# Kernel optimization log

Measured on AMD Instinct MI355X. Metric: run time of the kernel, lower is better.

The kernel has to match this reference:

```python
import jax, jax.numpy as jnp
import numpy as np

C = 512
NUM_GROUPS = 32
EPS = 1e-6


def group_norm(x, gamma, beta):
    # x: [B, C, H, W]
    B, Cc, H, W = x.shape
    xg = x.reshape(B, NUM_GROUPS, Cc // NUM_GROUPS, H, W)
    mean = xg.mean(axis=(2, 3, 4), keepdims=True)
    var = xg.var(axis=(2, 3, 4), keepdims=True)
    xn = (xg - mean) / jnp.sqrt(var + EPS)
    xn = xn.reshape(B, Cc, H, W)
    return xn * gamma[None, :, None, None] + beta[None, :, None, None]


def conv1x1(x, w, b):
    # w: [out_c, in_c], x: [B, C, H, W]
    return jnp.einsum('oc,bchw->bohw', w, x) + b[None, :, None, None]


def setup_inputs() -> dict:
    key = jax.random.key(0)
    ks = jax.random.split(key, 6)
    B, H, W = 2, 64, 64
    x = jax.random.normal(ks[0], (B, C, H, W), dtype=jnp.float32)
    s = 1.0 / np.sqrt(C)
    wq = jax.random.normal(ks[1], (C, C), dtype=jnp.float32) * s
    wk = jax.random.normal(ks[2], (C, C), dtype=jnp.float32) * s
    wv = jax.random.normal(ks[3], (C, C), dtype=jnp.float32) * s
    wo = jax.random.normal(ks[4], (C, C), dtype=jnp.float32) * s
    bq = jnp.zeros((C,), jnp.float32)
    bk = jnp.zeros((C,), jnp.float32)
    bv = jnp.zeros((C,), jnp.float32)
    bo = jnp.zeros((C,), jnp.float32)
    gamma = jnp.ones((C,), jnp.float32)
    beta = jnp.zeros((C,), jnp.float32)
    return {"x": x, "gamma": gamma, "beta": beta, "wq": wq, "bq": bq,
            "wk": wk, "bk": bk, "wv": wv, "bv": bv, "wo": wo, "bo": bo}


def reference(x, gamma, beta, wq, bq, wk, bk, wv, bv, wo, bo):
    B, Cc, H, W = x.shape
    h = group_norm(x, gamma, beta)
    q = conv1x1(h, wq, bq).reshape(B, Cc, H * W)  # [B, C, N]
    k = conv1x1(h, wk, bk).reshape(B, Cc, H * W)
    v = conv1x1(h, wv, bv).reshape(B, Cc, H * W)
    scale = Cc ** (-0.5)
    # scores a[b,i,j] = sum_c q[b,c,i] * k[b,c,j]
    a = jnp.einsum('bci,bcj->bij', q, k) * scale
    a = jax.nn.softmax(a, axis=2)
    # out[b,c,i] = sum_j v[b,c,j] * a[b,i,j]  (matches bmm(v, a^T))
    o = jnp.einsum('bcj,bij->bci', v, a).reshape(B, Cc, H, W)
    o = conv1x1(o, wo, bo)
    return x + o
```

## Files before the change

kernel.cpp:

```cpp
#include <hip/hip_runtime.h>
#include <stdint.h>

#define NPIX 4096
#define CDIM 512

typedef _Float16 hv8 __attribute__((ext_vector_type(8)));
typedef float f32x4 __attribute__((ext_vector_type(4)));

__device__ __forceinline__ void lds_direct16(const _Float16* g, _Float16* l) {
    __builtin_amdgcn_global_load_lds(
        (const __attribute__((address_space(1))) void*)g,
        (__attribute__((address_space(3))) void*)l, 16, 0, 0);
}

__global__ void cvt_w(const float* __restrict__ s0, const float* __restrict__ s1,
                      const float* __restrict__ s2, const float* __restrict__ s3,
                      _Float16* __restrict__ d0, _Float16* __restrict__ d1,
                      _Float16* __restrict__ d2, _Float16* __restrict__ d3) {
    int i = blockIdx.x * 256 + threadIdx.x;
    d0[i] = (_Float16)s0[i];
    d1[i] = (_Float16)s1[i];
    d2[i] = (_Float16)s2[i];
    d3[i] = (_Float16)s3[i];
}

__global__ void stats_kernel(const float* __restrict__ x, float* __restrict__ stats) {
    int idx = blockIdx.x;
    const float4* base = (const float4*)(x + (long)idx * 16 * NPIX);
    int tid = threadIdx.x;
    float s = 0.f, sq = 0.f;
    for (int it = 0; it < 64; ++it) {
        float4 f = base[it * 256 + tid];
        s  += f.x + f.y + f.z + f.w;
        sq += f.x * f.x + f.y * f.y + f.z * f.z + f.w * f.w;
    }
    __shared__ float rs[256], rq[256];
    rs[tid] = s; rq[tid] = sq;
    __syncthreads();
    for (int st = 128; st > 0; st >>= 1) {
        if (tid < st) { rs[tid] += rs[tid + st]; rq[tid] += rq[tid + st]; }
        __syncthreads();
    }
    if (tid == 0) {
        float mean = rs[0] * (1.0f / 65536.0f);
        float var  = rq[0] * (1.0f / 65536.0f) - mean * mean;
        stats[idx * 2]     = mean;
        stats[idx * 2 + 1] = rsqrtf(var + 1e-6f);
    }
}

__global__ void normT_kernel(const float* __restrict__ x, const float* __restrict__ stats,
                             const float* __restrict__ gamma, const float* __restrict__ beta,
                             _Float16* __restrict__ hT) {
    int b = blockIdx.z, c0 = blockIdx.x * 32, n0 = blockIdx.y * 32;
    int tid = threadIdx.x;
    __shared__ float t[32][33];
    int cl = tid >> 5;
    int nl = tid & 31;
    for (int r = 0; r < 4; ++r)
        t[r * 8 + cl][nl] = x[(long)b * CDIM * NPIX + (long)(c0 + r * 8 + cl) * NPIX + n0 + nl];
    __syncthreads();
    for (int r = 0; r < 4; ++r) {
        int nr = r * 8 + cl;
        int c = c0 + nl;
        float m    = stats[(b * 32 + (c >> 4)) * 2];
        float rstd = stats[(b * 32 + (c >> 4)) * 2 + 1];
        float val = (t[nl][nr] - m) * rstd * gamma[c] + beta[c];
        hT[(long)b * NPIX * CDIM + (long)(n0 + nr) * CDIM + c] = (_Float16)val;
    }
}

template<int EPI>
__launch_bounds__(256, 2)
__global__ void gemm_bt_kernel(const _Float16* __restrict__ A, const _Float16* __restrict__ BT,
                               void* __restrict__ D, const float* __restrict__ bias,
                               const float* __restrict__ resid,
                               int M, int N, int K,
                               long aBatch, long bBatch, long dBatch, long rBatch) {
    const int b = blockIdx.z;
    A  += (long)b * aBatch;
    BT += (long)b * bBatch;
    const int m0 = blockIdx.y * 128;
    const int n0 = blockIdx.x * 128;
    const int tid = threadIdx.x;
    const int l = tid & 63;
    const int w = tid >> 6;
    const int wm = (w >> 1) * 64;
    const int wn = (w & 1) * 64;
    const int lr = l & 15;
    const int lk = l >> 4;
    __shared__ __align__(16) _Float16 As[128 * 32];
    __shared__ __align__(16) _Float16 Bs[128 * 32];
    f32x4 acc[4][4] = {};
    const int nK = K >> 5;
    for (int kt = 0; kt < nK; ++kt) {
        const int kb = kt * 32;
#pragma unroll
        for (int c = 0; c < 2; ++c) {
            int chunk = c * 256 + tid;
            int row = chunk >> 2;
            int k8 = (chunk & 3) * 8;
            _Float16* ldsA = As + (size_t)(c * 256 + (tid & ~63)) * 8;
            _Float16* ldsB = Bs + (size_t)(c * 256 + (tid & ~63)) * 8;
            lds_direct16(A  + (long)(m0 + row) * K + kb + k8, ldsA);
            lds_direct16(BT + (long)(n0 + row) * K + kb + k8, ldsB);
        }
        __syncthreads();
        hv8 af[4], bfr[4];
#pragma unroll
        for (int mi = 0; mi < 4; ++mi)
            af[mi] = *(const hv8*)(As + (size_t)(wm + mi * 16 + lr) * 32 + lk * 8);
#pragma unroll
        for (int ni = 0; ni < 4; ++ni)
            bfr[ni] = *(const hv8*)(Bs + (size_t)(wn + ni * 16 + lr) * 32 + lk * 8);
#pragma unroll
        for (int mi = 0; mi < 4; ++mi)
#pragma unroll
            for (int ni = 0; ni < 4; ++ni)
                acc[mi][ni] = __builtin_amdgcn_mfma_f32_16x16x32_f16(af[mi], bfr[ni], acc[mi][ni], 0, 0, 0);
        __syncthreads();
    }
#pragma unroll
    for (int mi = 0; mi < 4; ++mi)
#pragma unroll
        for (int ni = 0; ni < 4; ++ni)
#pragma unroll
            for (int r = 0; r < 4; ++r) {
                int row = m0 + wm + mi * 16 + lk * 4 + r;
                int col = n0 + wn + ni * 16 + lr;
                float val = acc[mi][ni][r];
                if (EPI == 0) {
                    ((_Float16*)D)[(long)b * dBatch + (long)row * N + col] = (_Float16)(val + bias[col]);
                } else if (EPI == 1) {
                    ((_Float16*)D)[(long)b * dBatch + (long)row * N + col] = (_Float16)(val + bias[row]);
                } else {
                    long idx = (long)row * N + col;
                    ((float*)D)[(long)b * dBatch + idx] =
                        val + bias[row] + resid[(long)b * rBatch + idx];
                }
            }
}

__launch_bounds__(512, 2)
__global__ void attn_kernel(const _Float16* __restrict__ qT, const _Float16* __restrict__ kT,
                            const _Float16* __restrict__ v,
                            _Float16* __restrict__ p0, _Float16* __restrict__ p1,
                            float* __restrict__ lbuf) {
    __shared__ __align__(16) _Float16 Ks[2][32 * 512];
    __shared__ __align__(16) _Float16 Vs[2][512 * 32];
    __shared__ __align__(16) _Float16 ps[64 * 32];
    __shared__ float red[8][64];
    __shared__ float redt[64];

    const int g = blockIdx.x;
    const int xcd = g & 7;
    const int comb = xcd >> 1;
    const int itile = ((g >> 3) << 1) | (xcd & 1);
    const int batch = comb >> 1;
    const int jhalf = comb & 1;
    const int i0 = itile * 64;
    const int jbase = jhalf * 2048;

    const int tid = threadIdx.x;
    const int l = tid & 63, w = tid >> 6;
    const int lr = l & 15, lk = l >> 4;
    const int iq = w >> 1, jq = w & 1;

    const _Float16* qb = qT + (long)batch * NPIX * CDIM;
    const _Float16* kb = kT + (long)batch * NPIX * CDIM;
    const _Float16* vb = v  + (long)batch * CDIM * NPIX;

    hv8 af[16];
    {
        const _Float16* qr = qb + (long)(i0 + iq * 16 + lr) * CDIM + lk * 8;
#pragma unroll
        for (int kk = 0; kk < 16; ++kk)
            af[kk] = *(const hv8*)(qr + kk * 32);
    }

    f32x4 oacc[4][4] = {};
    float lsum[4] = {};

    const int vrow_lo = l >> 2;
    const int vslot   = (l & 3) ^ (vrow_lo & 3);

#define STAGE_TILE(buf, JJ)                                                          \
    {                                                                                \
        const long j0s = (JJ);                                                       \
        _Float16* kd = Ks[buf]; _Float16* vd = Vs[buf];                              \
        _Pragma("unroll")                                                            \
        for (int q = 0; q < 4; ++q) {                                                \
            int row = q * 8 + w;                                                     \
            int cc = l ^ (row & 7);                                                  \
            lds_direct16(kb + (j0s + row) * CDIM + cc * 8, kd + row * 512);          \
        }                                                                            \
        _Pragma("unroll")                                                            \
        for (int q = 0; q < 4; ++q) {                                                \
            int r16 = q * 8 + w;                                                     \
            int crow = r16 * 16 + vrow_lo;                                           \
            lds_direct16(vb + (long)crow * NPIX + j0s + vslot * 8, vd + r16 * 512);  \
        }                                                                            \
    }

    STAGE_TILE(0, (long)jbase)
    __syncthreads();

    const float scale = 0.044194173824159216f;

    for (int jt = 0; jt < 64; ++jt) {
        const int cur = jt & 1;

        if (jt < 63)
            STAGE_TILE(cur ^ 1, (long)jbase + (jt + 1) * 32)
        __builtin_amdgcn_sched_barrier(0);

        hv8 vf[4];
#pragma unroll
        for (int ni = 0; ni < 4; ++ni) {
            int c = w * 64 + ni * 16 + lr;
            uint32_t off = (uint32_t)(c * 64) + (((uint32_t)(lk * 16)) ^ ((uint32_t)((c & 3) << 4)));
            vf[ni] = *(const hv8*)((const char*)Vs[cur] + off);
        }

        f32x4 s = {};
        {
            const char* kbase = (const char*)Ks[cur];
            const int j = jq * 16 + lr;
            const uint32_t sw = (uint32_t)((j & 7) << 4);
#pragma unroll
            for (int kk = 0; kk < 16; ++kk) {
                hv8 bf = *(const hv8*)(kbase + (((uint32_t)(j * 1024 + kk * 64 + lk * 16)) ^ sw));
                s = __builtin_amdgcn_mfma_f32_16x16x32_f16(af[kk], bf, s, 0, 0, 0);
            }
        }

#pragma unroll
        for (int r = 0; r < 4; ++r) {
            float p = __expf(s[r] * scale);
            lsum[r] += p;
            int i = iq * 16 + lk * 4 + r;
            int j2 = jq * 16 + lr;
            uint32_t off = (uint32_t)(i * 64) + (((uint32_t)(j2 * 2)) ^ ((uint32_t)((i & 3) << 4)));
            *(_Float16*)((char*)ps + off) = (_Float16)p;
        }

        asm volatile("s_waitcnt lgkmcnt(0)" ::: "memory");
        __builtin_amdgcn_sched_barrier(0);
        __builtin_amdgcn_s_barrier();
        __builtin_amdgcn_sched_barrier(0);

#pragma unroll
        for (int mi = 0; mi < 4; ++mi) {
            int i2 = mi * 16 + lr;
            uint32_t off = (uint32_t)(i2 * 64) + (((uint32_t)(lk * 16)) ^ ((uint32_t)((i2 & 3) << 4)));
            hv8 pa = *(const hv8*)((const char*)ps + off);
#pragma unroll
            for (int ni = 0; ni < 4; ++ni)
                oacc[mi][ni] = __builtin_amdgcn_mfma_f32_16x16x32_f16(pa, vf[ni], oacc[mi][ni], 0, 0, 0);
        }

        __syncthreads();
    }

#pragma unroll
    for (int m = 1; m <= 8; m <<= 1)
#pragma unroll
        for (int r = 0; r < 4; ++r)
            lsum[r] += __shfl_xor(lsum[r], m, 64);
    if (lr == 0)
#pragma unroll
        for (int r = 0; r < 4; ++r)
            red[w][iq * 16 + lk * 4 + r] = lsum[r];
    __syncthreads();
    if (tid < 64) {
        int iq2 = tid >> 4;
        float lv = red[iq2 * 2][tid] + red[iq2 * 2 + 1][tid];
        redt[tid] = 1.0f / lv;
        lbuf[jhalf * 8192 + batch * NPIX + i0 + tid] = lv;
    }
    __syncthreads();

    _Float16* dsth = (jhalf ? p1 : p0) + (long)batch * NPIX * CDIM;
#pragma unroll
    for (int mi = 0; mi < 4; ++mi)
#pragma unroll
        for (int r = 0; r < 4; ++r) {
            int row = mi * 16 + lk * 4 + r;
            float rv = redt[row];
#pragma unroll
            for (int ni = 0; ni < 4; ++ni) {
                int c = w * 64 + ni * 16 + lr;
                dsth[(long)(i0 + row) * CDIM + c] = (_Float16)(oacc[mi][ni][r] * rv);
            }
        }
#undef STAGE_TILE
}

__global__ void combine_kernel(const _Float16* __restrict__ p0, const _Float16* __restrict__ p1,
                               const float* __restrict__ lbuf, _Float16* __restrict__ out) {
    long g = (long)blockIdx.x * 256 + threadIdx.x;
    long base = g * 8;
    int rowg = (int)(g >> 6);
    float l0 = lbuf[rowg], l1 = lbuf[8192 + rowg];
    float w0 = l0 / (l0 + l1);
    float w1 = 1.0f - w0;
    hv8 a = *(const hv8*)(p0 + base);
    hv8 b = *(const hv8*)(p1 + base);
    hv8 o;
#pragma unroll
    for (int i = 0; i < 8; ++i)
        o[i] = (_Float16)((float)a[i] * w0 + (float)b[i] * w1);
    *(hv8*)(out + base) = o;
}

extern "C" void kernel_launch(void* const* d_in, const int* in_sizes, int n_in,
                              void* d_out, int out_size, void* d_ws, size_t ws_size,
                              hipStream_t stream) {
    const float* x     = (const float*)d_in[0];
    const float* gamma = (const float*)d_in[1];
    const float* beta  = (const float*)d_in[2];
    const float* wq    = (const float*)d_in[3];
    const float* bq    = (const float*)d_in[4];
    const float* wk    = (const float*)d_in[5];
    const float* bk    = (const float*)d_in[6];
    const float* wv    = (const float*)d_in[7];
    const float* bv    = (const float*)d_in[8];
    const float* wo    = (const float*)d_in[9];
    const float* bo    = (const float*)d_in[10];
    float* out = (float*)d_out;

    char* ws = (char*)d_ws;
    float* stats = (float*)ws;
    _Float16* wqb = (_Float16*)(ws + 1024);
    _Float16* wkb = wqb + 262144;
    _Float16* wvb = wkb + 262144;
    _Float16* wob = wvb + 262144;
    _Float16* hT  = wob + 262144;
    const long TSZ = (long)2 * NPIX * CDIM;
    _Float16* qT = hT + TSZ;
    _Float16* kT = qT + TSZ;
    _Float16* vv = kT + TSZ;
    _Float16* oT = vv + TSZ;
    float* lbuf = (float*)(oT + TSZ);

    cvt_w<<<dim3(1024), dim3(256), 0, stream>>>(wq, wk, wv, wo, wqb, wkb, wvb, wob);
    stats_kernel<<<dim3(64), dim3(256), 0, stream>>>(x, stats);
    normT_kernel<<<dim3(16, 128, 2), dim3(256), 0, stream>>>(x, stats, gamma, beta, hT);

    const long NC = (long)NPIX * CDIM;
    gemm_bt_kernel<0><<<dim3(4, 32, 2), dim3(256), 0, stream>>>(
        hT, wqb, (void*)qT, bq, nullptr, NPIX, CDIM, CDIM, NC, 0L, NC, 0L);
    gemm_bt_kernel<0><<<dim3(4, 32, 2), dim3(256), 0, stream>>>(
        hT, wkb, (void*)kT, bk, nullptr, NPIX, CDIM, CDIM, NC, 0L, NC, 0L);
    gemm_bt_kernel<1><<<dim3(32, 4, 2), dim3(256), 0, stream>>>(
        wvb, hT, (void*)vv, bv, nullptr, CDIM, NPIX, CDIM, 0L, NC, NC, 0L);

    attn_kernel<<<dim3(256), dim3(512), 0, stream>>>(qT, kT, vv, oT, hT, lbuf);

    combine_kernel<<<dim3(2048), dim3(256), 0, stream>>>(oT, hT, lbuf, qT);

    gemm_bt_kernel<2><<<dim3(32, 4, 2), dim3(256), 0, stream>>>(
        wob, qT, (void*)out, bo, x, CDIM, NPIX, CDIM, 0L, NC, NC, NC);
}
```

Before: 206.2 us.

## Triple-buffer K tiles and load V straight into registers in attention loop

The attention kernel stops staging V through LDS and has each lane load its V fragments directly from global memory into registers, double-buffered across iterations. K tiles move to a three-deep LDS ring prefetched two steps ahead, with explicit vmcnt waits in place of the full trailing syncthreads. The QK dot product is split into two independent accumulators and the P tile swizzle is changed. The aim is to cut LDS traffic and barrier stalls and hide global latency better, at the cost of more registers and uncoalesced-looking V global loads.

```diff
diff --git a/kernel.cpp b/kernel.cpp
--- a/kernel.cpp
+++ b/kernel.cpp
@@ -146,8 +146,7 @@
                             const _Float16* __restrict__ v,
                             _Float16* __restrict__ p0, _Float16* __restrict__ p1,
                             float* __restrict__ lbuf) {
-    __shared__ __align__(16) _Float16 Ks[2][32 * 512];
-    __shared__ __align__(16) _Float16 Vs[2][512 * 32];
+    __shared__ __align__(16) _Float16 Ks[3][32 * 512];
     __shared__ __align__(16) _Float16 ps[64 * 32];
     __shared__ float red[8][64];
     __shared__ float redt[64];
@@ -180,86 +179,93 @@
 
     f32x4 oacc[4][4] = {};
     float lsum[4] = {};
-
-    const int vrow_lo = l >> 2;
-    const int vslot   = (l & 3) ^ (vrow_lo & 3);
-
-#define STAGE_TILE(buf, JJ)                                                          \
+    hv8 vfA[4], vfB[4];
+
+    const _Float16* vptr = vb + (long)(w * 64 + lr) * NPIX + jbase + lk * 8;
+    const float scale = 0.044194173824159216f;
+
+#define KSTAGE(JT)                                                                   \
     {                                                                                \
-        const long j0s = (JJ);                                                       \
-        _Float16* kd = Ks[buf]; _Float16* vd = Vs[buf];                              \
+        _Float16* kd = Ks[(JT) % 3];                                                 \
+        const _Float16* kpp = kb + (long)(jbase + (JT) * 32) * CDIM;                 \
         _Pragma("unroll")                                                            \
         for (int q = 0; q < 4; ++q) {                                                \
             int row = q * 8 + w;                                                     \
             int cc = l ^ (row & 7);                                                  \
-            lds_direct16(kb + (j0s + row) * CDIM + cc * 8, kd + row * 512);          \
-        }                                                                            \
-        _Pragma("unroll")                                                            \
-        for (int q = 0; q < 4; ++q) {                                                \
-            int r16 = q * 8 + w;                                                     \
-            int crow = r16 * 16 + vrow_lo;                                           \
-            lds_direct16(vb + (long)crow * NPIX + j0s + vslot * 8, vd + r16 * 512);  \
-        }                                                                            \
-    }
-
-    STAGE_TILE(0, (long)jbase)
-    __syncthreads();
-
-    const float scale = 0.044194173824159216f;
-
-    for (int jt = 0; jt < 64; ++jt) {
-        const int cur = jt & 1;
-
-        if (jt < 63)
-            STAGE_TILE(cur ^ 1, (long)jbase + (jt + 1) * 32)
-        __builtin_amdgcn_sched_barrier(0);
-
-        hv8 vf[4];
-#pragma unroll
-        for (int ni = 0; ni < 4; ++ni) {
-            int c = w * 64 + ni * 16 + lr;
-            uint32_t off = (uint32_t)(c * 64) + (((uint32_t)(lk * 16)) ^ ((uint32_t)((c & 3) << 4)));
-            vf[ni] = *(const hv8*)((const char*)Vs[cur] + off);
-        }
-
-        f32x4 s = {};
-        {
-            const char* kbase = (const char*)Ks[cur];
-            const int j = jq * 16 + lr;
-            const uint32_t sw = (uint32_t)((j & 7) << 4);
-#pragma unroll
-            for (int kk = 0; kk < 16; ++kk) {
-                hv8 bf = *(const hv8*)(kbase + (((uint32_t)(j * 1024 + kk * 64 + lk * 16)) ^ sw));
-                s = __builtin_amdgcn_mfma_f32_16x16x32_f16(af[kk], bf, s, 0, 0, 0);
-            }
-        }
-
-#pragma unroll
-        for (int r = 0; r < 4; ++r) {
-            float p = __expf(s[r] * scale);
-            lsum[r] += p;
-            int i = iq * 16 + lk * 4 + r;
-            int j2 = jq * 16 + lr;
-            uint32_t off = (uint32_t)(i * 64) + (((uint32_t)(j2 * 2)) ^ ((uint32_t)((i & 3) << 4)));
-            *(_Float16*)((char*)ps + off) = (_Float16)p;
-        }
-
-        asm volatile("s_waitcnt lgkmcnt(0)" ::: "memory");
-        __builtin_amdgcn_sched_barrier(0);
-        __builtin_amdgcn_s_barrier();
-        __builtin_amdgcn_sched_barrier(0);
-
-#pragma unroll
-        for (int mi = 0; mi < 4; ++mi) {
-            int i2 = mi * 16 + lr;
-            uint32_t off = (uint32_t)(i2 * 64) + (((uint32_t)(lk * 16)) ^ ((uint32_t)((i2 & 3) << 4)));
-            hv8 pa = *(const hv8*)((const char*)ps + off);
-#pragma unroll
-            for (int ni = 0; ni < 4; ++ni)
-                oacc[mi][ni] = __builtin_amdgcn_mfma_f32_16x16x32_f16(pa, vf[ni], oacc[mi][ni], 0, 0, 0);
-        }
-
-        __syncthreads();
+            lds_direct16(kpp + (long)row * CDIM + cc * 8, kd + row * 512);           \
+        }                                                                            \
+    }
+
+#define VLOAD(DST, JT)                                                               \
+    {                                                                                \
+        _Pragma("unroll")                                                            \
+        for (int ni = 0; ni < 4; ++ni)                                               \
+            DST[ni] = *(const hv8*)(vptr + (long)ni * (16 * NPIX) + (JT) * 32);      \
+    }
+
+#define STEP(JT, VFU, VFL)                                                           \
+    {                                                                                \
+        if ((JT) < 62) KSTAGE((JT) + 2)                                              \
+        __builtin_amdgcn_sched_barrier(0);                                           \
+        if ((JT) < 63) VLOAD(VFL, (JT) + 1)                                          \
+        __builtin_amdgcn_sched_barrier(0);                                           \
+                                         \
+        const char* kbase = (const char*)Ks[(JT) % 3];                               \
+        f32x4 sa = {}, sb = {};                                                      \
+        const int jj = jq * 16 + lr;                                                 \
+        const uint32_t sw = (uint32_t)((jj & 7) << 4);                               \
+        _Pragma("unroll")                                                            \
+        for (int kk = 0; kk < 8; ++kk) {                                             \
+            hv8 b0 = *(const hv8*)(kbase + (((uint32_t)(jj * 1024 + (2 * kk) * 64 + lk * 16)) ^ sw));     \
+            sa = __builtin_amdgcn_mfma_f32_16x16x32_f16(af[2 * kk], b0, sa, 0, 0, 0);                     \
+            hv8 b1 = *(const hv8*)(kbase + (((uint32_t)(jj * 1024 + (2 * kk + 1) * 64 + lk * 16)) ^ sw)); \
+            sb = __builtin_amdgcn_mfma_f32_16x16x32_f16(af[2 * kk + 1], b1, sb, 0, 0, 0);                 \
+        }                                                                            \
+        sa += sb;                                                                    \
+         \
+        _Pragma("unroll")                                                            \
+        for (int r = 0; r < 4; ++r) {                                                \
+            float p = __expf(sa[r] * scale);                                         \
+            lsum[r] += p;                                                            \
+            int i = iq * 16 + lk * 4 + r;                                            \
+            int slot = (jq * 2 + (lr >> 3)) ^ ((i >> 1) & 3);                        \
+            *(_Float16*)((char*)ps + i * 64 + slot * 16 + (lr & 7) * 2) = (_Float16)p; \
+        }                                                                            \
+                \
+        asm volatile("s_waitcnt lgkmcnt(0)" ::: "memory");                           \
+        __builtin_amdgcn_sched_barrier(0);                                           \
+        __builtin_amdgcn_s_barrier();                                                \
+        __builtin_amdgcn_sched_barrier(0);                                           \
+                                           \
+        _Pragma("unroll")                                                            \
+        for (int mi = 0; mi < 4; ++mi) {                                             \
+            int i2 = mi * 16 + lr;                                                   \
+            uint32_t off = (uint32_t)(i2 * 64 + ((lk ^ ((i2 >> 1) & 3)) << 4));      \
+            hv8 pa = *(const hv8*)((const char*)ps + off);                           \
+            _Pragma("unroll")                                                        \
+            for (int ni = 0; ni < 4; ++ni)                                           \
+                oacc[mi][ni] = __builtin_amdgcn_mfma_f32_16x16x32_f16(pa, VFU[ni], oacc[mi][ni], 0, 0, 0); \
+        }                                                                            \
+          \
+        if ((JT) < 63) {                                                             \
+            if ((JT) == 62) { asm volatile("s_waitcnt vmcnt(8)" ::: "memory"); }     \
+            else            { asm volatile("s_waitcnt vmcnt(12)" ::: "memory"); }    \
+            __builtin_amdgcn_sched_barrier(0);                                       \
+            __builtin_amdgcn_s_barrier();                                            \
+            __builtin_amdgcn_sched_barrier(0);                                       \
+        }                                                                            \
+    }
+
+    KSTAGE(0)
+    VLOAD(vfA, 0)
+    KSTAGE(1)
+    asm volatile("s_waitcnt vmcnt(12)" ::: "memory");
+    __builtin_amdgcn_s_barrier();
+    __builtin_amdgcn_sched_barrier(0);
+
+    for (int jt = 0; jt < 64; jt += 2) {
+        STEP(jt, vfA, vfB)
+        STEP(jt + 1, vfB, vfA)
     }
 
 #pragma unroll
@@ -293,7 +299,9 @@
                 dsth[(long)(i0 + row) * CDIM + c] = (_Float16)(oacc[mi][ni][r] * rv);
             }
         }
-#undef STAGE_TILE
+#undef STEP
+#undef VLOAD
+#undef KSTAGE
 }
 
 __global__ void combine_kernel(const _Float16* __restrict__ p0, const _Float16* __restrict__ p1,
```

After: 228.5 us. 1.11x slower.
